# Kernel tuning notes

Hardware: AMD Instinct MI355X
Metric: run time of the kernel (lower is better)

Reference implementation:

```python
import jax, jax.numpy as jnp
import numpy as np

GROUPS = 256   # == planes (default groups=None -> planes)
NODE_NUM = 32
EPS = 1e-5


def setup_inputs() -> dict:
    key = jax.random.key(0)
    ks = jax.random.split(key, 12)
    b, cin, planes, h, w = 4, 512, 256, 128, 128
    node_fea = planes // NODE_NUM  # 8
    inp = {
        "x": jax.random.normal(ks[0], (b, cin, h, w), jnp.float32),
        "Wt": jax.random.normal(ks[1], (planes, cin), jnp.float32) * 0.02,
        "Wp": jax.random.normal(ks[2], (planes, cin), jnp.float32) * 0.02,
        "Wg": jax.random.normal(ks[3], (planes, cin), jnp.float32) * 0.02,
        "Wz": jax.random.normal(ks[4], (cin,), jnp.float32) * 0.1,  # grouped 1x1 conv, 1 in-ch per group
        "W_adj": jax.random.normal(ks[5], (NODE_NUM, NODE_NUM), jnp.float32) * 0.1,
        "bn_adj_gamma": jnp.ones((NODE_NUM,), jnp.float32),
        "bn_adj_beta": jnp.zeros((NODE_NUM,), jnp.float32),
        "bn_adj_mean": jax.random.normal(ks[6], (NODE_NUM,), jnp.float32) * 0.1,
        "bn_adj_var": jax.random.uniform(ks[7], (NODE_NUM,), jnp.float32) + 0.5,
        "W_wg": jax.random.normal(ks[8], (node_fea, node_fea), jnp.float32) * 0.1,
        "bn_wg_gamma": jnp.ones((node_fea,), jnp.float32),
        "bn_wg_beta": jnp.zeros((node_fea,), jnp.float32),
        "bn_wg_mean": jax.random.normal(ks[9], (node_fea,), jnp.float32) * 0.1,
        "bn_wg_var": jax.random.uniform(ks[10], (node_fea,), jnp.float32) + 0.5,
        "gn_gamma": jnp.ones((cin,), jnp.float32),
        "gn_beta": jnp.zeros((cin,), jnp.float32),
    }
    return inp


def _bn1d_eval(z, mean, var, gamma, beta):
    # BatchNorm1d over channel dim 1 of [b, C, L], eval mode (running stats)
    inv = jax.lax.rsqrt(var + EPS)
    return (z - mean[:, None]) * (inv * gamma)[:, None] + beta[:, None]


def reference(x, Wt, Wp, Wg, Wz, W_adj, bn_adj_gamma, bn_adj_beta, bn_adj_mean,
              bn_adj_var, W_wg, bn_wg_gamma, bn_wg_beta, bn_wg_mean, bn_wg_var,
              gn_gamma, gn_beta):
    b, cin, h, w = x.shape
    # 1x1 convs t/p/g
    t = jnp.einsum('bihw,oi->bohw', x, Wt)
    p = jnp.einsum('bihw,oi->bohw', x, Wp)
    g = jnp.einsum('bihw,oi->bohw', x, Wg)
    planes = t.shape[1]
    node_fea = planes // NODE_NUM
    # per-group dot-product kernel: replaces the Python loop of tiny bmms.
    # _c = planes // GROUPS channels per group; att[b, gidx] = sum(p_g * g_g)
    att = jnp.sum((p * g).reshape(b, GROUPS, -1), axis=-1)  # [b, groups]
    # split(dim=1, node_num) + cat(dim=2): z_idt[b, i, k] = att[b, k*node_num + i]
    z_idt = att.reshape(b, GROUPS // NODE_NUM, NODE_NUM).transpose(0, 2, 1)  # [b, node_num, node_fea]
    # node-adjacency conv (Conv1d k=1 over node dim) + BN + ReLU + residual
    z = jnp.einsum('nm,bmf->bnf', W_adj, z_idt)
    z = _bn1d_eval(z, bn_adj_mean, bn_adj_var, bn_adj_gamma, bn_adj_beta)
    z = jax.nn.relu(z) + z_idt
    # feature conv on transposed layout + BN + ReLU
    z = z.transpose(0, 2, 1)  # [b, node_fea, node_num]
    z = jnp.einsum('fe,ben->bfn', W_wg, z)
    z = _bn1d_eval(z, bn_wg_mean, bn_wg_var, bn_wg_gamma, bn_wg_beta)
    z = jax.nn.relu(z).transpose(0, 2, 1)  # [b, node_num, node_fea]
    # reshape to per-channel scalars and gate t
    zvec = z.reshape(b, planes)[:, :, None, None]  # [b, planes, 1, 1]
    xg = zvec * t  # [b, planes, h, w]
    # grouped 1x1 conv z: groups=planes, 1 input ch / group, r=cin//planes out ch / group
    r = cin // planes
    y = Wz[None, :, None, None] * jnp.repeat(xg, r, axis=1)  # [b, cin, h, w]
    # GroupNorm(num_groups=GROUPS, num_channels=cin)
    yg = y.reshape(b, GROUPS, -1)  # each group: (cin//GROUPS)*h*w elements
    mean = yg.mean(axis=-1, keepdims=True)
    var = yg.var(axis=-1, keepdims=True)
    yn = ((yg - mean) * jax.lax.rsqrt(var + EPS)).reshape(b, cin, h, w)
    yn = yn * gn_gamma[None, :, None, None] + gn_beta[None, :, None, None]
    return yn + x
```

## Files before the change

kernel.cpp:

```cpp
#include <hip/hip_runtime.h>

#define HW 16384
#define CIN 512
#define PL 256
#define EPSF 1e-5f
#define SLO 0.0009765625f

using half8  = __attribute__((ext_vector_type(8))) _Float16;
using half4v = __attribute__((ext_vector_type(4))) _Float16;
using f32x4  = __attribute__((ext_vector_type(4))) float;

__device__ inline void gload_lds16(const void* g, void* l) {
  __builtin_amdgcn_global_load_lds((const __attribute__((address_space(1))) void*)g,
                                   (__attribute__((address_space(3))) void*)l, 16, 0, 0);
}

__global__ __launch_bounds__(256) void k_conv(const float* __restrict__ x,
                                              _Float16* __restrict__ Xh,
                                              _Float16* __restrict__ Xl,
                                              float* __restrict__ xsum) {
  __shared__ float ws4[4];
  int row = blockIdx.x;
  int tid = threadIdx.x;
  const float* xr = x + ((size_t)row << 14);
  _Float16* hr = Xh + ((size_t)row << 14);
  _Float16* lr = Xl + ((size_t)row << 14);
  float s = 0.f;
#pragma unroll
  for (int j = 0; j < 8; ++j) {
    int o = j * 2048 + tid * 8;
    float4 v0 = *reinterpret_cast<const float4*>(xr + o);
    float4 v1 = *reinterpret_cast<const float4*>(xr + o + 4);
    half8 h, l;
    h[0] = (_Float16)v0.x; h[1] = (_Float16)v0.y; h[2] = (_Float16)v0.z; h[3] = (_Float16)v0.w;
    h[4] = (_Float16)v1.x; h[5] = (_Float16)v1.y; h[6] = (_Float16)v1.z; h[7] = (_Float16)v1.w;
    l[0] = (_Float16)((v0.x - (float)h[0]) * 1024.f);
    l[1] = (_Float16)((v0.y - (float)h[1]) * 1024.f);
    l[2] = (_Float16)((v0.z - (float)h[2]) * 1024.f);
    l[3] = (_Float16)((v0.w - (float)h[3]) * 1024.f);
    l[4] = (_Float16)((v1.x - (float)h[4]) * 1024.f);
    l[5] = (_Float16)((v1.y - (float)h[5]) * 1024.f);
    l[6] = (_Float16)((v1.z - (float)h[6]) * 1024.f);
    l[7] = (_Float16)((v1.w - (float)h[7]) * 1024.f);
    *reinterpret_cast<half8*>(hr + o) = h;
    *reinterpret_cast<half8*>(lr + o) = l;
    s += v0.x + v0.y + v0.z + v0.w + v1.x + v1.y + v1.z + v1.w;
  }
#pragma unroll
  for (int m = 1; m < 64; m <<= 1) s += __shfl_xor(s, m);
  if ((tid & 63) == 0) ws4[tid >> 6] = s;
  __syncthreads();
  if (tid == 0) xsum[row] = ws4[0] + ws4[1] + ws4[2] + ws4[3];
}

__global__ __launch_bounds__(256) void k_xp16(const _Float16* __restrict__ Xh,
                                              _Float16* __restrict__ xT) {
  __shared__ _Float16 lds[64 * 72];
  int hw0 = blockIdx.x << 6;
  int c0 = blockIdx.y << 6;
  int b = blockIdx.z;
  int tid = threadIdx.x;
  int rl = tid >> 3, seg = tid & 7;
  const _Float16* hb = Xh + ((size_t)b << 23);
#pragma unroll
  for (int pass = 0; pass < 2; ++pass) {
    int cl = pass * 32 + rl;
    half8 v = *reinterpret_cast<const half8*>(hb + ((size_t)(c0 + cl) << 14) + hw0 + seg * 8);
#pragma unroll
    for (int e = 0; e < 8; ++e) lds[(seg * 8 + e) * 72 + cl] = v[e];
  }
  __syncthreads();
  _Float16* tb = xT + (((size_t)b << 14) + hw0) * CIN + c0;
#pragma unroll
  for (int pass = 0; pass < 2; ++pass) {
    int hwl = pass * 32 + rl;
    half8 o = *reinterpret_cast<const half8*>(&lds[hwl * 72 + seg * 8]);
    *reinterpret_cast<half8*>(tb + (size_t)hwl * CIN + seg * 8) = o;
  }
}

__global__ __launch_bounds__(256, 4) void k_gram(const _Float16* __restrict__ Xh,
                                                 const _Float16* __restrict__ Xl,
                                                 float* __restrict__ GH,
                                                 float* __restrict__ C1) {
  __shared__ _Float16 lA[128 * 64];
  __shared__ _Float16 lB[128 * 64];
  int wg = blockIdx.x;
  int id = (wg & 7) * 104 + (wg >> 3);
  int b = id / 208;
  int rem = id % 208;
  int ks = rem / 26;
  int u = rem % 26;
  int chain, ti, tj;
  if (u < 10) {
    chain = 0;
    ti = 0;
    while ((ti + 1) * (ti + 2) / 2 <= u) ++ti;
    tj = u - ti * (ti + 1) / 2;
  } else {
    chain = 1;
    int t = u - 10;
    ti = t >> 2; tj = t & 3;
  }
  int tid = threadIdx.x;
  int wave = tid >> 6, lane = tid & 63, l15 = lane & 15, l4 = lane >> 4;
  int wr = wave >> 1, wc = wave & 1;
  const _Float16* Asrc = (chain ? Xl : Xh) + (size_t)b * CIN * HW;
  const _Float16* Bsrc = Xh + (size_t)b * CIN * HW;
  float* D = chain ? C1 : GH;

  int srow = lane >> 3;
  int sgran = (lane & 7) ^ (srow & 7);
  int kbase = ks << 11;
  const _Float16* gA[4];
  const _Float16* gB[4];
#pragma unroll
  for (int i = 0; i < 4; ++i) {
    int row = i * 32 + wave * 8 + srow;
    gA[i] = Asrc + (size_t)(ti * 128 + row) * HW + kbase + sgran * 8;
    gB[i] = Bsrc + (size_t)(tj * 128 + row) * HW + kbase + sgran * 8;
  }
  char* ldA = (char*)lA + wave * 1024;
  char* ldB = (char*)lB + wave * 1024;

  int adA[4][2], adB[4][2];
#pragma unroll
  for (int rf = 0; rf < 4; ++rf) {
    int r = wr * 64 + rf * 16 + l15;
#pragma unroll
    for (int ksub = 0; ksub < 2; ++ksub)
      adA[rf][ksub] = r * 128 + (((ksub * 4 + l4) ^ (r & 7)) << 4);
  }
#pragma unroll
  for (int cf = 0; cf < 4; ++cf) {
    int c = wc * 64 + cf * 16 + l15;
#pragma unroll
    for (int ksub = 0; ksub < 2; ++ksub)
      adB[cf][ksub] = c * 128 + (((ksub * 4 + l4) ^ (c & 7)) << 4);
  }

  f32x4 acc[4][4];
#pragma unroll
  for (int rf = 0; rf < 4; ++rf)
#pragma unroll
    for (int cf = 0; cf < 4; ++cf) acc[rf][cf] = f32x4{0.f, 0.f, 0.f, 0.f};

  for (int s = 0; s < 32; ++s) {
    int ko = s * 64;
#pragma unroll
    for (int i = 0; i < 4; ++i) {
      gload_lds16(gA[i] + ko, ldA + i * 4096);
      gload_lds16(gB[i] + ko, ldB + i * 4096);
    }
    __syncthreads();
#pragma unroll
    for (int ksub = 0; ksub < 2; ++ksub) {
      half8 af[4], bf[4];
#pragma unroll
      for (int rf = 0; rf < 4; ++rf)
        af[rf] = *reinterpret_cast<const half8*>((char*)lA + adA[rf][ksub]);
#pragma unroll
      for (int cf = 0; cf < 4; ++cf)
        bf[cf] = *reinterpret_cast<const half8*>((char*)lB + adB[cf][ksub]);
#pragma unroll
      for (int rf = 0; rf < 4; ++rf)
#pragma unroll
        for (int cf = 0; cf < 4; ++cf)
          acc[rf][cf] = __builtin_amdgcn_mfma_f32_16x16x32_f16(af[rf], bf[cf], acc[rf][cf], 0, 0, 0);
    }
    __syncthreads();
  }

  size_t bo = (size_t)b << 18;
#pragma unroll
  for (int rf = 0; rf < 4; ++rf)
#pragma unroll
    for (int cf = 0; cf < 4; ++cf)
#pragma unroll
      for (int r = 0; r < 4; ++r) {
        int i = ti * 128 + wr * 64 + rf * 16 + l4 * 4 + r;
        int j = tj * 128 + wc * 64 + cf * 16 + l15;
        atomicAdd(D + bo + ((size_t)i << 9) + j, acc[rf][cf][r]);
      }
}

__global__ __launch_bounds__(256) void k_sym(const float* __restrict__ GH,
                                             const float* __restrict__ C1,
                                             float* __restrict__ Gs) {
  __shared__ float T1[64 * 65];
  __shared__ float TG[64 * 65];
  int I = blockIdx.x, J = blockIdx.y, b = blockIdx.z;
  int i0 = I << 6, j0 = J << 6;
  bool upper = (I >> 1) >= (J >> 1);
  size_t bo = (size_t)b << 18;
  int tid = threadIdx.x;
  int r = tid >> 2, cs = (tid & 3) << 4;
#pragma unroll
  for (int u = 0; u < 16; u += 4) {
    size_t toff = bo + (((size_t)(j0 + r)) << 9) + i0 + cs + u;
    float4 v = *reinterpret_cast<const float4*>(C1 + toff);
    T1[r * 65 + cs + u + 0] = v.x; T1[r * 65 + cs + u + 1] = v.y;
    T1[r * 65 + cs + u + 2] = v.z; T1[r * 65 + cs + u + 3] = v.w;
    if (!upper) {
      float4 g = *reinterpret_cast<const float4*>(GH + toff);
      TG[r * 65 + cs + u + 0] = g.x; TG[r * 65 + cs + u + 1] = g.y;
      TG[r * 65 + cs + u + 2] = g.z; TG[r * 65 + cs + u + 3] = g.w;
    }
  }
  __syncthreads();
#pragma unroll
  for (int u = 0; u < 16; u += 4) {
    size_t off = bo + (((size_t)(i0 + r)) << 9) + j0 + cs + u;
    float4 c = *reinterpret_cast<const float4*>(C1 + off);
    float t0 = T1[(cs + u + 0) * 65 + r];
    float t1 = T1[(cs + u + 1) * 65 + r];
    float t2 = T1[(cs + u + 2) * 65 + r];
    float t3 = T1[(cs + u + 3) * 65 + r];
    float4 o;
    if (upper) {
      float4 h = *reinterpret_cast<const float4*>(GH + off);
      o.x = h.x + SLO * (c.x + t0);
      o.y = h.y + SLO * (c.y + t1);
      o.z = h.z + SLO * (c.z + t2);
      o.w = h.w + SLO * (c.w + t3);
    } else {
      o.x = TG[(cs + u + 0) * 65 + r] + SLO * (c.x + t0);
      o.y = TG[(cs + u + 1) * 65 + r] + SLO * (c.y + t1);
      o.z = TG[(cs + u + 2) * 65 + r] + SLO * (c.z + t2);
      o.w = TG[(cs + u + 3) * 65 + r] + SLO * (c.w + t3);
    }
    *reinterpret_cast<float4*>(Gs + off) = o;
  }
}

__global__ __launch_bounds__(256) void k_V(const float* __restrict__ Gs,
                                           const float* __restrict__ Wg,
                                           const float* __restrict__ Wt,
                                           float* __restrict__ V) {
  __shared__ float Gl[64 * 65];
  __shared__ float Wl[64 * 65];
  int it = blockIdx.x, ot = blockIdx.y, b = blockIdx.z;
  int i0 = it << 6, o0 = ot << 6;
  int tid = threadIdx.x;
  int srow = tid >> 2, sseg = (tid & 3) << 4;
  const float* gsb = Gs + ((size_t)b << 18);
  int orow = o0 + srow;
  const float* wrow = (orow < 256) ? (Wg + (size_t)orow * 512) : (Wt + (size_t)(orow - 256) * 512);
  float acc[4][4];
#pragma unroll
  for (int a = 0; a < 4; ++a)
#pragma unroll
    for (int c = 0; c < 4; ++c) acc[a][c] = 0.f;
  int oy = (tid >> 4) << 2, ix = (tid & 15) << 2;
  for (int jc = 0; jc < 512; jc += 64) {
    __syncthreads();
#pragma unroll
    for (int u = 0; u < 16; u += 4) {
      float4 g = *reinterpret_cast<const float4*>(gsb + ((size_t)(i0 + srow) << 9) + jc + sseg + u);
      float4 w = *reinterpret_cast<const float4*>(wrow + jc + sseg + u);
      Gl[srow * 65 + sseg + u + 0] = g.x; Gl[srow * 65 + sseg + u + 1] = g.y;
      Gl[srow * 65 + sseg + u + 2] = g.z; Gl[srow * 65 + sseg + u + 3] = g.w;
      Wl[srow * 65 + sseg + u + 0] = w.x; Wl[srow * 65 + sseg + u + 1] = w.y;
      Wl[srow * 65 + sseg + u + 2] = w.z; Wl[srow * 65 + sseg + u + 3] = w.w;
    }
    __syncthreads();
    for (int j = 0; j < 64; ++j) {
      float w0 = Wl[(oy + 0) * 65 + j], w1 = Wl[(oy + 1) * 65 + j];
      float w2 = Wl[(oy + 2) * 65 + j], w3 = Wl[(oy + 3) * 65 + j];
      float g0 = Gl[(ix + 0) * 65 + j], g1 = Gl[(ix + 1) * 65 + j];
      float g2 = Gl[(ix + 2) * 65 + j], g3 = Gl[(ix + 3) * 65 + j];
      acc[0][0] += w0 * g0; acc[0][1] += w0 * g1; acc[0][2] += w0 * g2; acc[0][3] += w0 * g3;
      acc[1][0] += w1 * g0; acc[1][1] += w1 * g1; acc[1][2] += w1 * g2; acc[1][3] += w1 * g3;
      acc[2][0] += w2 * g0; acc[2][1] += w2 * g1; acc[2][2] += w2 * g2; acc[2][3] += w2 * g3;
      acc[3][0] += w3 * g0; acc[3][1] += w3 * g1; acc[3][2] += w3 * g2; acc[3][3] += w3 * g3;
    }
  }
  float* vb = V + ((size_t)b << 18);
#pragma unroll
  for (int a = 0; a < 4; ++a) {
    float4 vv = {acc[a][0], acc[a][1], acc[a][2], acc[a][3]};
    *reinterpret_cast<float4*>(vb + ((size_t)(o0 + oy + a) << 9) + i0 + ix) = vv;
  }
}

__global__ __launch_bounds__(256) void k_red2(const float* __restrict__ V,
                                              const float* __restrict__ xsum,
                                              const float* __restrict__ Wp,
                                              const float* __restrict__ Wt,
                                              float* __restrict__ att,
                                              float* __restrict__ tsum,
                                              float* __restrict__ tsq) {
  int blk = blockIdx.x;
  int b = blk >> 4;
  int og = (blk & 15) << 4;
  int tid = threadIdx.x;
  int ol = tid >> 4, seg = tid & 15;
  int o = og + ol;
  const float* vg = V + ((size_t)b << 18) + ((size_t)o << 9) + seg * 32;
  const float* vt = V + ((size_t)b << 18) + ((size_t)(256 + o) << 9) + seg * 32;
  const float* wp = Wp + (size_t)o * 512 + seg * 32;
  const float* wt = Wt + (size_t)o * 512 + seg * 32;
  const float* xs = xsum + b * CIN + seg * 32;
  float sa = 0.f, sq = 0.f, sm = 0.f;
#pragma unroll
  for (int i = 0; i < 32; i += 4) {
    float4 a = *reinterpret_cast<const float4*>(vg + i);
    float4 p = *reinterpret_cast<const float4*>(wp + i);
    float4 c = *reinterpret_cast<const float4*>(vt + i);
    float4 t = *reinterpret_cast<const float4*>(wt + i);
    float4 s = *reinterpret_cast<const float4*>(xs + i);
    sa += a.x * p.x + a.y * p.y + a.z * p.z + a.w * p.w;
    sq += c.x * t.x + c.y * t.y + c.z * t.z + c.w * t.w;
    sm += t.x * s.x + t.y * s.y + t.z * s.z + t.w * s.w;
  }
#pragma unroll
  for (int m = 1; m < 16; m <<= 1) {
    sa += __shfl_xor(sa, m);
    sq += __shfl_xor(sq, m);
    sm += __shfl_xor(sm, m);
  }
  if (seg == 0) {
    att[b * PL + o] = sa;
    tsq[b * PL + o] = sq;
    tsum[b * PL + o] = sm;
  }
}

__global__ __launch_bounds__(1024) void k_graph(
    const float* __restrict__ att, const float* __restrict__ tsum, const float* __restrict__ tsq,
    const float* __restrict__ W_adj, const float* __restrict__ bnag, const float* __restrict__ bnab,
    const float* __restrict__ bnam, const float* __restrict__ bnav,
    const float* __restrict__ W_wg, const float* __restrict__ bwgg, const float* __restrict__ bwgb,
    const float* __restrict__ bwgm, const float* __restrict__ bwgv,
    const float* __restrict__ Wz, const float* __restrict__ gng, const float* __restrict__ gnb,
    float* __restrict__ sA, float* __restrict__ sB) {
  __shared__ float att_l[4 * 256];
  __shared__ float z_l[4 * 256];
  __shared__ float zv_l[4 * 256];
  int tid = threadIdx.x;
  att_l[tid] = att[tid];
  __syncthreads();
  int b = tid >> 8, r = tid & 255, i = r >> 3, k = r & 7;
  float z1 = 0.f;
#pragma unroll
  for (int m = 0; m < 32; ++m) z1 += W_adj[i * 32 + m] * att_l[b * 256 + k * 32 + m];
  float inv = rsqrtf(bnav[i] + EPSF);
  float z = (z1 - bnam[i]) * inv * bnag[i] + bnab[i];
  z = fmaxf(z, 0.f) + att_l[b * 256 + k * 32 + i];
  z_l[b * 256 + i * 8 + k] = z;
  __syncthreads();
  float z2 = 0.f;
#pragma unroll
  for (int e = 0; e < 8; ++e) z2 += W_wg[k * 8 + e] * z_l[b * 256 + i * 8 + e];
  float inv2 = rsqrtf(bwgv[k] + EPSF);
  z2 = (z2 - bwgm[k]) * inv2 * bwgg[k] + bwgb[k];
  zv_l[b * 256 + i * 8 + k] = fmaxf(z2, 0.f);
  __syncthreads();
  int g = r;
  float s = zv_l[b * 256 + g];
  float m1 = tsum[b * 256 + g] * (1.f / 16384.f);
  float m2 = tsq[b * 256 + g] * (1.f / 16384.f);
  float a0 = Wz[2 * g] * s, a1 = Wz[2 * g + 1] * s;
  float mu = 0.5f * (a0 + a1) * m1;
  float ey2 = 0.5f * (a0 * a0 + a1 * a1) * m2;
  float var = ey2 - mu * mu;
  float invg = rsqrtf(var + EPSF);
  int c = b * CIN + 2 * g;
  sA[c]     = a0 * invg * gng[2 * g];
  sA[c + 1] = a1 * invg * gng[2 * g + 1];
  sB[c]     = gnb[2 * g]     - mu * invg * gng[2 * g];
  sB[c + 1] = gnb[2 * g + 1] - mu * invg * gng[2 * g + 1];
}

__global__ __launch_bounds__(256) void k_M(const float* __restrict__ Wt,
                                           const float* __restrict__ sA,
                                           _Float16* __restrict__ M) {
  int idx = blockIdx.x * 256 + threadIdx.x;
  int k8 = idx & 63;
  int c = (idx >> 6) & 511;
  int b = idx >> 15;
  float s = sA[b * 512 + c];
  const float* wrow = Wt + ((size_t)(c >> 1) << 9) + k8 * 8;
  int kbase = k8 * 8;
  half8 h;
#pragma unroll
  for (int j = 0; j < 8; ++j) {
    float v = s * wrow[j] + ((kbase + j) == c ? 1.f : 0.f);
    h[j] = (_Float16)v;
  }
  *reinterpret_cast<half8*>(M + (((size_t)(b * 512 + c)) << 9) + kbase) = h;
}

__global__ __launch_bounds__(256, 4) void k_tout(const _Float16* __restrict__ xT,
                                                 const _Float16* __restrict__ M,
                                                 const float* __restrict__ sB,
                                                 float* __restrict__ out) {
  __shared__ _Float16 lA[128 * 32];
  __shared__ _Float16 lB[128 * 32];
  int wg = blockIdx.x;
  int id = (wg & 7) * 256 + (wg >> 3);
  int b = id >> 9;
  int rem = id & 511;
  int ct = rem >> 7;
  int ht = rem & 127;
  int tid = threadIdx.x;
  int wave = tid >> 6, lane = tid & 63, l15 = lane & 15, l4 = lane >> 4;
  int wr = wave >> 1, wc = wave & 1;
  const _Float16* Mb = M + ((size_t)b << 18);
  const _Float16* xTb = xT + (size_t)b * HW * CIN;

  int srow = lane >> 2;
  int gran = (lane & 3) ^ ((srow >> 1) & 3);
  const _Float16* gA[2];
  const _Float16* gB[2];
#pragma unroll
  for (int i = 0; i < 2; ++i) {
    int row = i * 64 + wave * 16 + srow;
    gA[i] = Mb + ((size_t)(ct * 128 + row) << 9) + gran * 8;
    gB[i] = xTb + ((size_t)(ht * 128 + row) << 9) + gran * 8;
  }
  char* ldA = (char*)lA + wave * 1024;
  char* ldB = (char*)lB + wave * 1024;

  int adA[4], adB[4];
#pragma unroll
  for (int rf = 0; rf < 4; ++rf) {
    int r = wr * 64 + rf * 16 + l15;
    adA[rf] = r * 64 + ((l4 ^ ((r >> 1) & 3)) << 4);
  }
#pragma unroll
  for (int cf = 0; cf < 4; ++cf) {
    int c = wc * 64 + cf * 16 + l15;
    adB[cf] = c * 64 + ((l4 ^ ((c >> 1) & 3)) << 4);
  }

  f32x4 acc[4][4];
#pragma unroll
  for (int rf = 0; rf < 4; ++rf)
#pragma unroll
    for (int cf = 0; cf < 4; ++cf) acc[rf][cf] = f32x4{0.f, 0.f, 0.f, 0.f};

  for (int s = 0; s < 16; ++s) {
    int ko = s * 32;
    gload_lds16(gA[0] + ko, ldA);
    gload_lds16(gA[1] + ko, ldA + 4096);
    gload_lds16(gB[0] + ko, ldB);
    gload_lds16(gB[1] + ko, ldB + 4096);
    __syncthreads();
    half8 af[4], bf[4];
#pragma unroll
    for (int rf = 0; rf < 4; ++rf) af[rf] = *reinterpret_cast<const half8*>((char*)lA + adA[rf]);
#pragma unroll
    for (int cf = 0; cf < 4; ++cf) bf[cf] = *reinterpret_cast<const half8*>((char*)lB + adB[cf]);
#pragma unroll
    for (int rf = 0; rf < 4; ++rf)
#pragma unroll
      for (int cf = 0; cf < 4; ++cf)
        acc[rf][cf] = __builtin_amdgcn_mfma_f32_16x16x32_f16(af[rf], bf[cf], acc[rf][cf], 0, 0, 0);
    __syncthreads();
  }

  size_t outb = ((size_t)b * CIN) << 14;
#pragma unroll
  for (int rf = 0; rf < 4; ++rf) {
#pragma unroll
    for (int r = 0; r < 4; ++r) {
      int c = ct * 128 + wr * 64 + rf * 16 + l4 * 4 + r;
      float bb = sB[b * CIN + c];
      size_t off = outb + ((size_t)c << 14) + ht * 128 + wc * 64 + l15;
#pragma unroll
      for (int cf = 0; cf < 4; ++cf)
        out[off + cf * 16] = acc[rf][cf][r] + bb;
    }
  }
}

extern "C" void kernel_launch(void* const* d_in, const int* in_sizes, int n_in,
                              void* d_out, int out_size, void* d_ws, size_t ws_size,
                              hipStream_t stream) {
  const float* x    = (const float*)d_in[0];
  const float* Wt   = (const float*)d_in[1];
  const float* Wp   = (const float*)d_in[2];
  const float* Wg   = (const float*)d_in[3];
  const float* Wz   = (const float*)d_in[4];
  const float* Wadj = (const float*)d_in[5];
  const float* bnag = (const float*)d_in[6];
  const float* bnab = (const float*)d_in[7];
  const float* bnam = (const float*)d_in[8];
  const float* bnav = (const float*)d_in[9];
  const float* Wwg  = (const float*)d_in[10];
  const float* bwgg = (const float*)d_in[11];
  const float* bwgb = (const float*)d_in[12];
  const float* bwgm = (const float*)d_in[13];
  const float* bwgv = (const float*)d_in[14];
  const float* gng  = (const float*)d_in[15];
  const float* gnb  = (const float*)d_in[16];

  char* ws = (char*)d_ws;
  _Float16* xT = (_Float16*)(ws);
  float* GH   = (float*)(ws + 67371008);
  float* C1   = (float*)(ws + 71565312);
  float* Gs   = (float*)(ws + 75759616);
  float* V    = (float*)(ws + 79953920);
  float* xsum = (float*)(ws + 84148224);
  float* att  = (float*)(ws + 84156416);
  float* tsum = (float*)(ws + 84160512);
  float* tsq  = (float*)(ws + 84164608);
  float* sA   = (float*)(ws + 84168704);
  float* sB   = (float*)(ws + 84176896);
  if (ws_size < (size_t)84185088) return;
  _Float16* M = (_Float16*)GH;

  _Float16* Xh = (_Float16*)((char*)d_out);
  _Float16* Xl = (_Float16*)((char*)d_out + 67108864);
  float* out = (float*)d_out;

  hipMemsetAsync(GH, 0, 8388608, stream);
  k_conv<<<dim3(2048), dim3(256), 0, stream>>>(x, Xh, Xl, xsum);
  k_xp16<<<dim3(256, 8, 4), dim3(256), 0, stream>>>(Xh, xT);
  k_gram<<<dim3(832), dim3(256), 0, stream>>>(Xh, Xl, GH, C1);
  k_sym<<<dim3(8, 8, 4), dim3(256), 0, stream>>>(GH, C1, Gs);
  k_V<<<dim3(8, 8, 4), dim3(256), 0, stream>>>(Gs, Wg, Wt, V);
  k_red2<<<dim3(64), dim3(256), 0, stream>>>(V, xsum, Wp, Wt, att, tsum, tsq);
  k_graph<<<dim3(1), dim3(1024), 0, stream>>>(att, tsum, tsq, Wadj, bnag, bnab, bnam, bnav,
                                              Wwg, bwgg, bwgb, bwgm, bwgv, Wz, gng, gnb, sA, sB);
  k_M<<<dim3(512), dim3(256), 0, stream>>>(Wt, sA, M);
  k_tout<<<dim3(2048), dim3(256), 0, stream>>>(xT, M, sB, out);
}
```

Measured before the change: 289.4 us.

## Double-buffer LDS in gram and output GEMMs, split gram K further

Both MFMA GEMM kernels (k_gram and k_tout) get double-buffered LDS tiles. The next K-slice is issued with global_load_lds while the current slice is computed, which aims to hide global memory latency behind the MFMA work. k_gram also halves its K-chunk per block and doubles the grid to 1664 blocks, giving more parallelism at the cost of more atomic-style partial accumulation traffic. The gram kernel's LDS use doubles to 64KB, so launch bounds drop to 2 blocks per CU. The loop keeps a single barrier per iteration, which raises a question of whether the buffer being overwritten is properly synchronized (the trailing sync inside the loop presumably remains).

```diff
diff --git a/kernel.cpp b/kernel.cpp
--- a/kernel.cpp
+++ b/kernel.cpp
@@ -79,16 +79,15 @@
   }
 }
 
-__global__ __launch_bounds__(256, 4) void k_gram(const _Float16* __restrict__ Xh,
+__global__ __launch_bounds__(256, 2) void k_gram(const _Float16* __restrict__ Xh,
                                                  const _Float16* __restrict__ Xl,
                                                  float* __restrict__ GH,
                                                  float* __restrict__ C1) {
-  __shared__ _Float16 lA[128 * 64];
-  __shared__ _Float16 lB[128 * 64];
+  __shared__ _Float16 lds[2][2][128 * 64];
   int wg = blockIdx.x;
-  int id = (wg & 7) * 104 + (wg >> 3);
-  int b = id / 208;
-  int rem = id % 208;
+  int id = (wg & 7) * 208 + (wg >> 3);
+  int b = id / 416;
+  int rem = id % 416;
   int ks = rem / 26;
   int u = rem % 26;
   int chain, ti, tj;
@@ -111,7 +110,7 @@
 
   int srow = lane >> 3;
   int sgran = (lane & 7) ^ (srow & 7);
-  int kbase = ks << 11;
+  int kbase = ks << 10;
   const _Float16* gA[4];
   const _Float16* gB[4];
 #pragma unroll
@@ -120,8 +119,6 @@
     gA[i] = Asrc + (size_t)(ti * 128 + row) * HW + kbase + sgran * 8;
     gB[i] = Bsrc + (size_t)(tj * 128 + row) * HW + kbase + sgran * 8;
   }
-  char* ldA = (char*)lA + wave * 1024;
-  char* ldB = (char*)lB + wave * 1024;
 
   int adA[4][2], adB[4][2];
 #pragma unroll
@@ -145,23 +142,39 @@
 #pragma unroll
     for (int cf = 0; cf < 4; ++cf) acc[rf][cf] = f32x4{0.f, 0.f, 0.f, 0.f};
 
-  for (int s = 0; s < 32; ++s) {
-    int ko = s * 64;
+  {
+    char* dA = (char*)lds[0][0] + wave * 1024;
+    char* dB = (char*)lds[0][1] + wave * 1024;
 #pragma unroll
     for (int i = 0; i < 4; ++i) {
-      gload_lds16(gA[i] + ko, ldA + i * 4096);
-      gload_lds16(gB[i] + ko, ldB + i * 4096);
-    }
-    __syncthreads();
+      gload_lds16(gA[i], dA + i * 4096);
+      gload_lds16(gB[i], dB + i * 4096);
+    }
+  }
+  __syncthreads();
+
+  for (int s = 0; s < 16; ++s) {
+    if (s + 1 < 16) {
+      int ko = (s + 1) * 64;
+      char* dA = (char*)lds[(s + 1) & 1][0] + wave * 1024;
+      char* dB = (char*)lds[(s + 1) & 1][1] + wave * 1024;
+#pragma unroll
+      for (int i = 0; i < 4; ++i) {
+        gload_lds16(gA[i] + ko, dA + i * 4096);
+        gload_lds16(gB[i] + ko, dB + i * 4096);
+      }
+    }
+    char* cA = (char*)lds[s & 1][0];
+    char* cB = (char*)lds[s & 1][1];
 #pragma unroll
     for (int ksub = 0; ksub < 2; ++ksub) {
       half8 af[4], bf[4];
 #pragma unroll
       for (int rf = 0; rf < 4; ++rf)
-        af[rf] = *reinterpret_cast<const half8*>((char*)lA + adA[rf][ksub]);
+        af[rf] = *reinterpret_cast<const half8*>(cA + adA[rf][ksub]);
 #pragma unroll
       for (int cf = 0; cf < 4; ++cf)
-        bf[cf] = *reinterpret_cast<const half8*>((char*)lB + adB[cf][ksub]);
+        bf[cf] = *reinterpret_cast<const half8*>(cB + adB[cf][ksub]);
 #pragma unroll
       for (int rf = 0; rf < 4; ++rf)
 #pragma unroll
@@ -395,8 +408,7 @@
                                                  const _Float16* __restrict__ M,
                                                  const float* __restrict__ sB,
                                                  float* __restrict__ out) {
-  __shared__ _Float16 lA[128 * 32];
-  __shared__ _Float16 lB[128 * 32];
+  __shared__ _Float16 lds[2][2][128 * 32];
   int wg = blockIdx.x;
   int id = (wg & 7) * 256 + (wg >> 3);
   int b = id >> 9;
@@ -419,8 +431,6 @@
     gA[i] = Mb + ((size_t)(ct * 128 + row) << 9) + gran * 8;
     gB[i] = xTb + ((size_t)(ht * 128 + row) << 9) + gran * 8;
   }
-  char* ldA = (char*)lA + wave * 1024;
-  char* ldB = (char*)lB + wave * 1024;
 
   int adA[4], adB[4];
 #pragma unroll
@@ -440,18 +450,33 @@
 #pragma unroll
     for (int cf = 0; cf < 4; ++cf) acc[rf][cf] = f32x4{0.f, 0.f, 0.f, 0.f};
 
+  {
+    char* dA = (char*)lds[0][0] + wave * 1024;
+    char* dB = (char*)lds[0][1] + wave * 1024;
+    gload_lds16(gA[0], dA);
+    gload_lds16(gA[1], dA + 4096);
+    gload_lds16(gB[0], dB);
+    gload_lds16(gB[1], dB + 4096);
+  }
+  __syncthreads();
+
   for (int s = 0; s < 16; ++s) {
-    int ko = s * 32;
-    gload_lds16(gA[0] + ko, ldA);
-    gload_lds16(gA[1] + ko, ldA + 4096);
-    gload_lds16(gB[0] + ko, ldB);
-    gload_lds16(gB[1] + ko, ldB + 4096);
-    __syncthreads();
+    if (s + 1 < 16) {
+      int ko = (s + 1) * 32;
+      char* dA = (char*)lds[(s + 1) & 1][0] + wave * 1024;
+      char* dB = (char*)lds[(s + 1) & 1][1] + wave * 1024;
+      gload_lds16(gA[0] + ko, dA);
+      gload_lds16(gA[1] + ko, dA + 4096);
+      gload_lds16(gB[0] + ko, dB);
+      gload_lds16(gB[1] + ko, dB + 4096);
+    }
+    char* cA = (char*)lds[s & 1][0];
+    char* cB = (char*)lds[s & 1][1];
     half8 af[4], bf[4];
 #pragma unroll
-    for (int rf = 0; rf < 4; ++rf) af[rf] = *reinterpret_cast<const half8*>((char*)lA + adA[rf]);
-#pragma unroll
-    for (int cf = 0; cf < 4; ++cf) bf[cf] = *reinterpret_cast<const half8*>((char*)lB + adB[cf]);
+    for (int rf = 0; rf < 4; ++rf) af[rf] = *reinterpret_cast<const half8*>(cA + adA[rf]);
+#pragma unroll
+    for (int cf = 0; cf < 4; ++cf) bf[cf] = *reinterpret_cast<const half8*>(cB + adB[cf]);
 #pragma unroll
     for (int rf = 0; rf < 4; ++rf)
 #pragma unroll
@@ -518,7 +543,7 @@
   hipMemsetAsync(GH, 0, 8388608, stream);
   k_conv<<<dim3(2048), dim3(256), 0, stream>>>(x, Xh, Xl, xsum);
   k_xp16<<<dim3(256, 8, 4), dim3(256), 0, stream>>>(Xh, xT);
-  k_gram<<<dim3(832), dim3(256), 0, stream>>>(Xh, Xl, GH, C1);
+  k_gram<<<dim3(1664), dim3(256), 0, stream>>>(Xh, Xl, GH, C1);
   k_sym<<<dim3(8, 8, 4), dim3(256), 0, stream>>>(GH, C1, Gs);
   k_V<<<dim3(8, 8, 4), dim3(256), 0, stream>>>(Gs, Wg, Wt, V);
   k_red2<<<dim3(64), dim3(256), 0, stream>>>(V, xsum, Wp, Wt, att, tsum, tsq);
```

After: 307.4 us. 6.2% more time.
